# Kernel tuning notes

Measured on AMD Instinct MI355X. Metric: run time of the kernel, lower is better.

Reference implementation:

```python
import jax, jax.numpy as jnp
import numpy as np

B, S, D, H = 4, 2048, 1024, 16
HD = D // H  # head dim = 64


def setup_inputs() -> dict:
    key = jax.random.key(0)
    ks = jax.random.split(key, 11)
    sc = 1.0 / np.sqrt(D)
    return {
        "q": jax.random.normal(ks[0], (B, S, D), jnp.float32),
        "k": jax.random.normal(ks[1], (B, S, D), jnp.float32),
        "v": jax.random.normal(ks[2], (B, S, D), jnp.float32),
        "w_q": jax.random.normal(ks[3], (D, D), jnp.float32) * sc,
        "b_q": jnp.zeros((D,), jnp.float32),
        "w_k": jax.random.normal(ks[4], (D, D), jnp.float32) * sc,
        "b_k": jnp.zeros((D,), jnp.float32),
        "w_v": jax.random.normal(ks[5], (D, D), jnp.float32) * sc,
        "b_v": jnp.zeros((D,), jnp.float32),
        "w_fc": jax.random.normal(ks[6], (D, D), jnp.float32) * sc,
        "b_fc": jnp.zeros((D,), jnp.float32),
    }


def reference(q, k, v, w_q, b_q, w_k, b_k, w_v, b_v, w_fc, b_fc):
    scale = jnp.asarray(np.sqrt(HD), q.dtype)
    # QKV projections: [B,S,D] @ [D,D]^T (torch Linear: x @ W^T + b)
    Q = (q @ w_q.T + b_q).reshape(B, S, H, HD).transpose(0, 2, 1, 3)  # [B,H,S,HD]
    K = (k @ w_k.T + b_k).reshape(B, S, H, HD).transpose(0, 2, 1, 3)
    V = (v @ w_v.T + b_v).reshape(B, S, H, HD).transpose(0, 2, 1, 3)
    energy = jnp.einsum('bhqd,bhkd->bhqk', Q, K) / scale  # [B,H,S,S]
    attn = jax.nn.softmax(energy, axis=-1)  # dropout is identity in eval / p=0
    x = jnp.einsum('bhqk,bhkd->bhqd', attn, V)  # [B,H,S,HD]
    x = x.transpose(0, 2, 1, 3).reshape(B, S, D)
    return x @ w_fc.T + b_fc
```

## Files before the change

### kernel.cpp

```cpp
#include <hip/hip_runtime.h>
#include <stdint.h>

#define BN 4
#define SEQ 2048
#define DM 1024
#define NH 16
#define HD 64
#define ROWS (BN*SEQ)

typedef float  f32x4  __attribute__((ext_vector_type(4)));
typedef __bf16 bf16x8 __attribute__((ext_vector_type(8)));
typedef __bf16 bf16x4 __attribute__((ext_vector_type(4)));

#define QSCALE 0.18033688f

__device__ inline bf16x8 cvt8(const float* __restrict__ src) {
    float4 x0 = *(const float4*)src;
    float4 x1 = *(const float4*)(src + 4);
    bf16x8 r;
    r[0] = (__bf16)x0.x; r[1] = (__bf16)x0.y; r[2] = (__bf16)x0.z; r[3] = (__bf16)x0.w;
    r[4] = (__bf16)x1.x; r[5] = (__bf16)x1.y; r[6] = (__bf16)x1.z; r[7] = (__bf16)x1.w;
    return r;
}

__device__ inline void gl_lds16(const void* g, void* l) {
    __builtin_amdgcn_global_load_lds((const __attribute__((address_space(1))) uint32_t*)g,
                                     (__attribute__((address_space(3))) uint32_t*)l, 16, 0, 0);
}

__global__ __launch_bounds__(256) void cast3(
    const float* __restrict__ a0, const float* __restrict__ a1, const float* __restrict__ a2,
    __bf16* __restrict__ o0, __bf16* __restrict__ o1, __bf16* __restrict__ o2, int n8) {
    int t = blockIdx.x * 256 + threadIdx.x;
    if (t >= n8) return;
    const float* in = (blockIdx.y == 0) ? a0 : (blockIdx.y == 1) ? a1 : a2;
    __bf16* out     = (blockIdx.y == 0) ? o0 : (blockIdx.y == 1) ? o1 : o2;
    *(bf16x8*)&out[(size_t)t * 8] = cvt8(&in[(size_t)t * 8]);
}

__global__ __launch_bounds__(256) void cast4(
    const float* __restrict__ a0, const float* __restrict__ a1,
    const float* __restrict__ a2, const float* __restrict__ a3,
    __bf16* __restrict__ o0, __bf16* __restrict__ o1,
    __bf16* __restrict__ o2, __bf16* __restrict__ o3, int n8) {
    int t = blockIdx.x * 256 + threadIdx.x;
    if (t >= n8) return;
    const float* in = (blockIdx.y == 0) ? a0 : (blockIdx.y == 1) ? a1 : (blockIdx.y == 2) ? a2 : a3;
    __bf16* out     = (blockIdx.y == 0) ? o0 : (blockIdx.y == 1) ? o1 : (blockIdx.y == 2) ? o2 : o3;
    *(bf16x8*)&out[(size_t)t * 8] = cvt8(&in[(size_t)t * 8]);
}

#define GEMM_CORE_GLDS(Xp, Wp)                                                     \
    __shared__ __align__(16) __bf16 As[128 * 32];                                  \
    __shared__ __align__(16) __bf16 Bs[128 * 32];                                  \
    const int tid  = threadIdx.x;                                                  \
    const int lane = tid & 63;                                                     \
    const int wave = tid >> 6;                                                     \
    const int wm = (wave >> 1) * 64;                                               \
    const int wn = (wave & 1) * 64;                                                \
    const int c16 = lane & 15;                                                     \
    const int g8  = (lane >> 4) * 8;                                               \
    const int row0 = blockIdx.x * 128;                                             \
    const int col0 = blockIdx.y * 128;                                             \
    f32x4 acc[4][4] = {};                                                          \
    for (int k0 = 0; k0 < DM; k0 += 32) {                                          \
        __syncthreads();                                                           \
        _Pragma("unroll")                                                          \
        for (int h = 0; h < 2; h++) {                                              \
            int cidx = h * 256 + tid;                                              \
            gl_lds16(&Xp[(size_t)(row0 + (cidx >> 2)) * DM + k0 + (cidx & 3) * 8], \
                     &As[(size_t)(h * 256 + wave * 64) * 8]);                      \
            gl_lds16(&Wp[(size_t)(col0 + (cidx >> 2)) * DM + k0 + (cidx & 3) * 8], \
                     &Bs[(size_t)(h * 256 + wave * 64) * 8]);                      \
        }                                                                          \
        __syncthreads();                                                           \
        bf16x8 a[4], bfr[4];                                                       \
        _Pragma("unroll")                                                          \
        for (int i = 0; i < 4; i++) a[i]   = *(const bf16x8*)&As[(wm + i * 16 + c16) * 32 + g8]; \
        _Pragma("unroll")                                                          \
        for (int i = 0; i < 4; i++) bfr[i] = *(const bf16x8*)&Bs[(wn + i * 16 + c16) * 32 + g8]; \
        _Pragma("unroll")                                                          \
        for (int mi = 0; mi < 4; mi++)                                             \
            _Pragma("unroll")                                                      \
            for (int ni = 0; ni < 4; ni++)                                         \
                acc[mi][ni] = __builtin_amdgcn_mfma_f32_16x16x32_bf16(a[mi], bfr[ni], acc[mi][ni], 0, 0, 0); \
    }

__global__ __launch_bounds__(256) void gemm_qkv_f(
    const __bf16* __restrict__ qb, const __bf16* __restrict__ kb,
    const __bf16* __restrict__ vb,
    const __bf16* __restrict__ wqb, const __bf16* __restrict__ wkb,
    const __bf16* __restrict__ wvb,
    const float* __restrict__ bq, const float* __restrict__ bk,
    const float* __restrict__ bv,
    __bf16* __restrict__ Qp, __bf16* __restrict__ Kp, __bf16* __restrict__ Vt)
{
    const int z = blockIdx.z;
    const __bf16* X = (z == 0) ? qb : (z == 1) ? kb : vb;
    const __bf16* W = (z == 0) ? wqb : (z == 1) ? wkb : wvb;
    const float* bias = (z == 0) ? bq : (z == 1) ? bk : bv;

    GEMM_CORE_GLDS(X, W)

    if (z < 2) {
        __bf16* O = z ? Kp : Qp;
        const float qsc = z ? 1.0f : QSCALE;
        #pragma unroll
        for (int mi = 0; mi < 4; mi++) {
            int r0 = row0 + wm + mi * 16 + (lane >> 4) * 4;
            #pragma unroll
            for (int ni = 0; ni < 4; ni++) {
                int col = col0 + wn + ni * 16 + c16;
                float bsv = bias[col];
                int h = col >> 6, d = col & 63;
                #pragma unroll
                for (int i = 0; i < 4; i++) {
                    int r = r0 + i; int b = r >> 11, s = r & 2047;
                    O[((size_t)(b * NH + h) * SEQ + s) * HD + d] = (__bf16)((acc[mi][ni][i] + bsv) * qsc);
                }
            }
        }
    } else {
        #pragma unroll
        for (int mi = 0; mi < 4; mi++) {
            int r0 = row0 + wm + mi * 16 + (lane >> 4) * 4;
            #pragma unroll
            for (int ni = 0; ni < 4; ni++) {
                int col = col0 + wn + ni * 16 + c16;
                float bsv = bias[col];
                int h = col >> 6, d = col & 63;
                int b = r0 >> 11, s0 = r0 & 2047;
                size_t base = ((size_t)((b * NH + h) * HD + d)) * SEQ + s0;
                #pragma unroll
                for (int i = 0; i < 4; i++)
                    Vt[base + i] = (__bf16)(acc[mi][ni][i] + bsv);
            }
        }
    }
}

__global__ __launch_bounds__(256) void gemm_fc_f(
    const __bf16* __restrict__ Xc, const __bf16* __restrict__ Wfb,
    const float* __restrict__ bias, float* __restrict__ out)
{
    __shared__ __align__(16) __bf16 As[128 * 32];
    __shared__ __align__(16) __bf16 Bs[64 * 32];

    const int tid  = threadIdx.x;
    const int lane = tid & 63;
    const int wave = tid >> 6;
    const int wm = (wave >> 1) * 64;
    const int wn = (wave & 1) * 32;
    const int c16 = lane & 15;
    const int g8  = (lane >> 4) * 8;
    const int row0 = blockIdx.x * 128;
    const int col0 = blockIdx.y * 64;

    f32x4 acc[4][2] = {};
    for (int k0 = 0; k0 < DM; k0 += 32) {
        __syncthreads();
        #pragma unroll
        for (int h = 0; h < 2; h++) {
            int cidx = h * 256 + tid;
            gl_lds16(&Xc[(size_t)(row0 + (cidx >> 2)) * DM + k0 + (cidx & 3) * 8],
                     &As[(size_t)(h * 256 + wave * 64) * 8]);
        }
        gl_lds16(&Wfb[(size_t)(col0 + (tid >> 2)) * DM + k0 + (tid & 3) * 8],
                 &Bs[(size_t)(wave * 64) * 8]);
        __syncthreads();

        bf16x8 a[4], bfr[2];
        #pragma unroll
        for (int i = 0; i < 4; i++) a[i]   = *(const bf16x8*)&As[(wm + i * 16 + c16) * 32 + g8];
        #pragma unroll
        for (int i = 0; i < 2; i++) bfr[i] = *(const bf16x8*)&Bs[(wn + i * 16 + c16) * 32 + g8];
        #pragma unroll
        for (int mi = 0; mi < 4; mi++)
            #pragma unroll
            for (int ni = 0; ni < 2; ni++)
                acc[mi][ni] = __builtin_amdgcn_mfma_f32_16x16x32_bf16(a[mi], bfr[ni], acc[mi][ni], 0, 0, 0);
    }

    #pragma unroll
    for (int mi = 0; mi < 4; mi++) {
        int r0 = row0 + wm + mi * 16 + (lane >> 4) * 4;
        #pragma unroll
        for (int ni = 0; ni < 2; ni++) {
            int col = col0 + wn + ni * 16 + c16;
            float bsv = bias[col];
            #pragma unroll
            for (int i = 0; i < 4; i++)
                out[(size_t)(r0 + i) * DM + col] = acc[mi][ni][i] + bsv;
        }
    }
}

__global__ __launch_bounds__(256) void gemm_qk(
    const __bf16* __restrict__ qb, const __bf16* __restrict__ kb,
    const float* __restrict__ wqf, const float* __restrict__ wkf,
    const float* __restrict__ bq, const float* __restrict__ bk,
    __bf16* __restrict__ Qp, __bf16* __restrict__ Kp)
{
    const int z = blockIdx.z;
    const __bf16* X = z ? kb : qb;
    const float* W  = z ? wkf : wqf;
    const float* bias = z ? bk : bq;
    __bf16* O = z ? Kp : Qp;
    const float qsc = z ? 1.0f : QSCALE;

    __shared__ __align__(16) __bf16 As[128 * 32];
    __shared__ __align__(16) __bf16 Bs[128 * 32];

    const int tid  = threadIdx.x;
    const int lane = tid & 63;
    const int wave = tid >> 6;
    const int wm = (wave >> 1) * 64;
    const int wn = (wave & 1) * 64;
    const int c16 = lane & 15;
    const int g8  = (lane >> 4) * 8;
    const int row0 = blockIdx.x * 128;
    const int col0 = blockIdx.y * 128;
    const int brow = tid >> 1;
    const int bcc  = (tid & 1) * 16;

    f32x4 acc[4][4] = {};
    for (int k0 = 0; k0 < DM; k0 += 32) {
        __syncthreads();
        #pragma unroll
        for (int h = 0; h < 2; h++) {
            int cidx = h * 256 + tid;
            gl_lds16(&X[(size_t)(row0 + (cidx >> 2)) * DM + k0 + (cidx & 3) * 8],
                     &As[(size_t)(h * 256 + wave * 64) * 8]);
        }
        *(bf16x8*)&Bs[brow * 32 + bcc]     = cvt8(&W[(size_t)(col0 + brow) * DM + k0 + bcc]);
        *(bf16x8*)&Bs[brow * 32 + bcc + 8] = cvt8(&W[(size_t)(col0 + brow) * DM + k0 + bcc + 8]);
        __syncthreads();

        bf16x8 a[4], bfr[4];
        #pragma unroll
        for (int i = 0; i < 4; i++) a[i]   = *(const bf16x8*)&As[(wm + i * 16 + c16) * 32 + g8];
        #pragma unroll
        for (int i = 0; i < 4; i++) bfr[i] = *(const bf16x8*)&Bs[(wn + i * 16 + c16) * 32 + g8];
        #pragma unroll
        for (int mi = 0; mi < 4; mi++)
            #pragma unroll
            for (int ni = 0; ni < 4; ni++)
                acc[mi][ni] = __builtin_amdgcn_mfma_f32_16x16x32_bf16(a[mi], bfr[ni], acc[mi][ni], 0, 0, 0);
    }

    #pragma unroll
    for (int mi = 0; mi < 4; mi++) {
        int r0 = row0 + wm + mi * 16 + (lane >> 4) * 4;
        #pragma unroll
        for (int ni = 0; ni < 4; ni++) {
            int col = col0 + wn + ni * 16 + c16;
            float bsv = bias[col];
            int h = col >> 6, d = col & 63;
            #pragma unroll
            for (int i = 0; i < 4; i++) {
                int r = r0 + i; int b = r >> 11, s = r & 2047;
                O[((size_t)(b * NH + h) * SEQ + s) * HD + d] = (__bf16)((acc[mi][ni][i] + bsv) * qsc);
            }
        }
    }
}

__global__ __launch_bounds__(256) void gemm_v(
    const float* __restrict__ vf, const float* __restrict__ wvf,
    const float* __restrict__ bv, __bf16* __restrict__ Vt)
{
    __shared__ __align__(16) __bf16 As[128 * 32];
    __shared__ __align__(16) __bf16 Bs[128 * 32];

    const int tid  = threadIdx.x;
    const int lane = tid & 63;
    const int wave = tid >> 6;
    const int wm = (wave >> 1) * 64;
    const int wn = (wave & 1) * 64;
    const int c16 = lane & 15;
    const int g8  = (lane >> 4) * 8;
    const int row0 = blockIdx.x * 128;
    const int col0 = blockIdx.y * 128;
    const int brow = tid >> 1;
    const int bcc  = (tid & 1) * 16;

    f32x4 acc[4][4] = {};
    for (int k0 = 0; k0 < DM; k0 += 32) {
        __syncthreads();
        *(bf16x8*)&As[brow * 32 + bcc]     = cvt8(&vf[(size_t)(row0 + brow) * DM + k0 + bcc]);
        *(bf16x8*)&As[brow * 32 + bcc + 8] = cvt8(&vf[(size_t)(row0 + brow) * DM + k0 + bcc + 8]);
        *(bf16x8*)&Bs[brow * 32 + bcc]     = cvt8(&wvf[(size_t)(col0 + brow) * DM + k0 + bcc]);
        *(bf16x8*)&Bs[brow * 32 + bcc + 8] = cvt8(&wvf[(size_t)(col0 + brow) * DM + k0 + bcc + 8]);
        __syncthreads();

        bf16x8 a[4], bfr[4];
        #pragma unroll
        for (int i = 0; i < 4; i++) a[i]   = *(const bf16x8*)&As[(wm + i * 16 + c16) * 32 + g8];
        #pragma unroll
        for (int i = 0; i < 4; i++) bfr[i] = *(const bf16x8*)&Bs[(wn + i * 16 + c16) * 32 + g8];
        #pragma unroll
        for (int mi = 0; mi < 4; mi++)
            #pragma unroll
            for (int ni = 0; ni < 4; ni++)
                acc[mi][ni] = __builtin_amdgcn_mfma_f32_16x16x32_bf16(a[mi], bfr[ni], acc[mi][ni], 0, 0, 0);
    }

    #pragma unroll
    for (int mi = 0; mi < 4; mi++) {
        int r0 = row0 + wm + mi * 16 + (lane >> 4) * 4;
        #pragma unroll
        for (int ni = 0; ni < 4; ni++) {
            int col = col0 + wn + ni * 16 + c16;
            float bsv = bv[col];
            int h = col >> 6, d = col & 63;
            int b = r0 >> 11, s0 = r0 & 2047;
            size_t base = ((size_t)((b * NH + h) * HD + d)) * SEQ + s0;
            #pragma unroll
            for (int i = 0; i < 4; i++)
                Vt[base + i] = (__bf16)(acc[mi][ni][i] + bsv);
        }
    }
}

__global__ __launch_bounds__(256) void gemm_fc(
    const __bf16* __restrict__ Xc, const float* __restrict__ Wf,
    const float* __restrict__ bias, float* __restrict__ out)
{
    __shared__ __align__(16) __bf16 As[128 * 32];
    __shared__ __align__(16) __bf16 Bs[128 * 32];

    const int tid  = threadIdx.x;
    const int lane = tid & 63;
    const int wave = tid >> 6;
    const int wm = (wave >> 1) * 64;
    const int wn = (wave & 1) * 64;
    const int c16 = lane & 15;
    const int g8  = (lane >> 4) * 8;
    const int row0 = blockIdx.x * 128;
    const int col0 = blockIdx.y * 128;
    const int brow = tid >> 1;
    const int bcc  = (tid & 1) * 16;

    f32x4 acc[4][4] = {};
    for (int k0 = 0; k0 < DM; k0 += 32) {
        __syncthreads();
        #pragma unroll
        for (int h = 0; h < 2; h++) {
            int cidx = h * 256 + tid;
            gl_lds16(&Xc[(size_t)(row0 + (cidx >> 2)) * DM + k0 + (cidx & 3) * 8],
                     &As[(size_t)(h * 256 + wave * 64) * 8]);
        }
        *(bf16x8*)&Bs[brow * 32 + bcc]     = cvt8(&Wf[(size_t)(col0 + brow) * DM + k0 + bcc]);
        *(bf16x8*)&Bs[brow * 32 + bcc + 8] = cvt8(&Wf[(size_t)(col0 + brow) * DM + k0 + bcc + 8]);
        __syncthreads();

        bf16x8 a[4], bfr[4];
        #pragma unroll
        for (int i = 0; i < 4; i++) a[i]   = *(const bf16x8*)&As[(wm + i * 16 + c16) * 32 + g8];
        #pragma unroll
        for (int i = 0; i < 4; i++) bfr[i] = *(const bf16x8*)&Bs[(wn + i * 16 + c16) * 32 + g8];
        #pragma unroll
        for (int mi = 0; mi < 4; mi++)
            #pragma unroll
            for (int ni = 0; ni < 4; ni++)
                acc[mi][ni] = __builtin_amdgcn_mfma_f32_16x16x32_bf16(a[mi], bfr[ni], acc[mi][ni], 0, 0, 0);
    }

    #pragma unroll
    for (int mi = 0; mi < 4; mi++) {
        int r0 = row0 + wm + mi * 16 + (lane >> 4) * 4;
        #pragma unroll
        for (int ni = 0; ni < 4; ni++) {
            int col = col0 + wn + ni * 16 + c16;
            float bsv = bias[col];
            #pragma unroll
            for (int i = 0; i < 4; i++)
                out[(size_t)(r0 + i) * DM + col] = acc[mi][ni][i] + bsv;
        }
    }
}

__global__ __launch_bounds__(256, 4) void attn_kernel(
    const __bf16* __restrict__ Qp, const __bf16* __restrict__ Kp,
    const __bf16* __restrict__ Vt, __bf16* __restrict__ ctx)
{
    __shared__ __align__(16) __bf16 Ks[2][64 * 64];
    __shared__ __align__(16) __bf16 Vs[2][64 * 64];

    const int tid  = threadIdx.x;
    const int lane = tid & 63;
    const int w    = tid >> 6;
    const int bh   = blockIdx.x;
    const int q0   = blockIdx.y * 128 + w * 32;

    const __bf16* Qb = Qp + (size_t)bh * SEQ * HD;
    const __bf16* Kb = Kp + (size_t)bh * SEQ * HD;
    const __bf16* Vb = Vt + (size_t)bh * HD * SEQ;

    const int c16 = lane & 15;
    const int g   = lane >> 4;
    const int sw  = c16 & 7;

    bf16x8 qf[2][2];
    #pragma unroll
    for (int qs = 0; qs < 2; qs++)
        #pragma unroll
        for (int kc = 0; kc < 2; kc++)
            qf[qs][kc] = *(const bf16x8*)&Qb[(size_t)(q0 + qs * 16 + c16) * HD + kc * 32 + g * 8];

    float lp[2] = {0.f, 0.f};
    f32x4 o[4][2] = {};

    const int srow = (w * 16) + (lane >> 3);
    const int sj   = (lane & 7) ^ (lane >> 3);

    auto stage = [&](int kt, int buf) {
        const int k0 = kt * 64;
        #pragma unroll
        for (int h = 0; h < 2; h++) {
            int r = srow + h * 8;
            gl_lds16(&Kb[(size_t)(k0 + r) * HD + sj * 8], &Ks[buf][(size_t)(w * 16 + h * 8) * 64]);
            gl_lds16(&Vb[(size_t)r * SEQ + k0 + sj * 8],  &Vs[buf][(size_t)(w * 16 + h * 8) * 64]);
        }
    };

    const int NT = SEQ / 64;
    stage(0, 0);
    int cur = 0;

    for (int kt = 0; kt < NT; kt++) {
        __syncthreads();
        if (kt + 1 < NT) stage(kt + 1, cur ^ 1);

        const __bf16* ksb = &Ks[cur][0];
        const __bf16* vsb = &Vs[cur][0];

        f32x4 sc[4][2] = {};
        #pragma unroll
        for (int t = 0; t < 4; t++) {
            #pragma unroll
            for (int kc = 0; kc < 2; kc++) {
                bf16x8 kf = *(const bf16x8*)&ksb[(t * 16 + c16) * 64 + ((kc * 4 + g) ^ sw) * 8];
                sc[t][0] = __builtin_amdgcn_mfma_f32_16x16x32_bf16(kf, qf[0][kc], sc[t][0], 0, 0, 0);
                sc[t][1] = __builtin_amdgcn_mfma_f32_16x16x32_bf16(kf, qf[1][kc], sc[t][1], 0, 0, 0);
            }
        }

        bf16x8 pf[2][2];
        #pragma unroll
        for (int qs = 0; qs < 2; qs++) {
            float ps = 0.f;
            #pragma unroll
            for (int kc = 0; kc < 2; kc++) {
                bf16x8 pv8;
                #pragma unroll
                for (int i = 0; i < 4; i++) {
                    float pv = exp2f(sc[2 * kc][qs][i]);
                    ps += pv; pv8[i] = (__bf16)pv;
                }
                #pragma unroll
                for (int i = 0; i < 4; i++) {
                    float pv = exp2f(sc[2 * kc + 1][qs][i]);
                    ps += pv; pv8[4 + i] = (__bf16)pv;
                }
                pf[qs][kc] = pv8;
            }
            lp[qs] += ps;
        }

        #pragma unroll
        for (int t = 0; t < 4; t++) {
            #pragma unroll
            for (int kc = 0; kc < 2; kc++) {
                union { bf16x8 v8; bf16x4 v4[2]; } u;
                u.v4[0] = *(const bf16x4*)&vsb[(t * 16 + c16) * 64 + (((kc * 4 + (g >> 1)) ^ sw) * 8) + (g & 1) * 4];
                u.v4[1] = *(const bf16x4*)&vsb[(t * 16 + c16) * 64 + (((kc * 4 + 2 + (g >> 1)) ^ sw) * 8) + (g & 1) * 4];
                o[t][0] = __builtin_amdgcn_mfma_f32_16x16x32_bf16(u.v8, pf[0][kc], o[t][0], 0, 0, 0);
                o[t][1] = __builtin_amdgcn_mfma_f32_16x16x32_bf16(u.v8, pf[1][kc], o[t][1], 0, 0, 0);
            }
        }

        cur ^= 1;
    }

    const int hh = bh & (NH - 1);
    const int bb = bh >> 4;
    #pragma unroll
    for (int qs = 0; qs < 2; qs++) {
        float l = lp[qs];
        l += __shfl_xor(l, 16, 64);
        l += __shfl_xor(l, 32, 64);
        float inv = 1.f / l;
        int s = q0 + qs * 16 + c16;
        #pragma unroll
        for (int t = 0; t < 4; t++) {
            bf16x4 ov;
            #pragma unroll
            for (int i = 0; i < 4; i++) ov[i] = (__bf16)(o[t][qs][i] * inv);
            *(bf16x4*)&ctx[((size_t)(bb * SEQ + s)) * DM + hh * HD + t * 16 + g * 4] = ov;
        }
    }
}

extern "C" void kernel_launch(void* const* d_in, const int* in_sizes, int n_in,
                              void* d_out, int out_size, void* d_ws, size_t ws_size,
                              hipStream_t stream) {
    const float* q    = (const float*)d_in[0];
    const float* k    = (const float*)d_in[1];
    const float* v    = (const float*)d_in[2];
    const float* w_q  = (const float*)d_in[3];
    const float* b_q  = (const float*)d_in[4];
    const float* w_k  = (const float*)d_in[5];
    const float* b_k  = (const float*)d_in[6];
    const float* w_v  = (const float*)d_in[7];
    const float* b_v  = (const float*)d_in[8];
    const float* w_fc = (const float*)d_in[9];
    const float* b_fc = (const float*)d_in[10];
    float* out = (float*)d_out;

    __bf16* qb = (__bf16*)d_out;
    __bf16* kb = qb + (size_t)ROWS * DM;

    char* p = (char*)d_ws;
    auto alloc = [&](size_t bytes) { char* r = p; p += (bytes + 255) & ~(size_t)255; return r; };
    const size_t XSZ = (size_t)ROWS * DM * 2;
    const size_t WSZ = (size_t)DM * DM * 2;

    __bf16* Qp  = (__bf16*)alloc(XSZ);
    __bf16* Kp  = (__bf16*)alloc(XSZ);
    __bf16* Vt  = (__bf16*)alloc(XSZ);
    __bf16* ctx = (__bf16*)alloc(XSZ);

    const size_t base_need = (size_t)(p - (char*)d_ws);
    const size_t fast_need = base_need + 4 * (WSZ + 256);

    const int n8x = ROWS * DM / 8;
    const int n8w = DM * DM / 8;

    __bf16* vb = ctx;

    cast3<<<dim3(n8x / 256, 3), 256, 0, stream>>>(q, k, v, qb, kb, vb, n8x);

    if (ws_size >= fast_need) {
        __bf16* wqb  = (__bf16*)alloc(WSZ);
        __bf16* wkb  = (__bf16*)alloc(WSZ);
        __bf16* wvb  = (__bf16*)alloc(WSZ);
        __bf16* wfcb = (__bf16*)alloc(WSZ);

        cast4<<<dim3(n8w / 256, 4), 256, 0, stream>>>(
            w_q, w_k, w_v, w_fc, wqb, wkb, wvb, wfcb, n8w);

        gemm_qkv_f<<<dim3(ROWS / 128, DM / 128, 3), 256, 0, stream>>>(
            qb, kb, vb, wqb, wkb, wvb, b_q, b_k, b_v, Qp, Kp, Vt);

        attn_kernel<<<dim3(BN * NH, SEQ / 128), 256, 0, stream>>>(Qp, Kp, Vt, ctx);

        gemm_fc_f<<<dim3(ROWS / 128, DM / 64), 256, 0, stream>>>(ctx, wfcb, b_fc, out);
    } else {
        gemm_v<<<dim3(ROWS / 128, DM / 128), 256, 0, stream>>>(v, w_v, b_v, Vt);
        gemm_qk<<<dim3(ROWS / 128, DM / 128, 2), 256, 0, stream>>>(
            qb, kb, w_q, w_k, b_q, b_k, Qp, Kp);

        attn_kernel<<<dim3(BN * NH, SEQ / 128), 256, 0, stream>>>(Qp, Kp, Vt, ctx);

        gemm_fc<<<dim3(ROWS / 128, DM / 128), 256, 0, stream>>>(ctx, w_fc, b_fc, out);
    }
}
```

Before: 360.2 us.

## Software-pipeline attention: overlap next tile's QK MFMA with current softmax/PV

```diff
diff --git a/kernel.cpp b/kernel.cpp
--- a/kernel.cpp
+++ b/kernel.cpp
@@ -380,7 +380,61 @@
     }
 }
 
-__global__ __launch_bounds__(256, 4) void attn_kernel(
+#define QK_CLUSTER(SC, KSB)                                                        \
+    do {                                                                           \
+        _Pragma("unroll")                                                          \
+        for (int t_ = 0; t_ < 4; t_++) {                                           \
+            SC[t_][0] = (f32x4){0.f, 0.f, 0.f, 0.f};                               \
+            SC[t_][1] = (f32x4){0.f, 0.f, 0.f, 0.f};                               \
+        }                                                                          \
+        _Pragma("unroll")                                                          \
+        for (int t_ = 0; t_ < 4; t_++) {                                           \
+            _Pragma("unroll")                                                      \
+            for (int kc = 0; kc < 2; kc++) {                                       \
+                bf16x8 kf = *(const bf16x8*)&(KSB)[(t_ * 16 + c16) * 64 + ((kc * 4 + g) ^ sw) * 8]; \
+                SC[t_][0] = __builtin_amdgcn_mfma_f32_16x16x32_bf16(kf, qf[0][kc], SC[t_][0], 0, 0, 0); \
+                SC[t_][1] = __builtin_amdgcn_mfma_f32_16x16x32_bf16(kf, qf[1][kc], SC[t_][1], 0, 0, 0); \
+            }                                                                      \
+        }                                                                          \
+    } while (0)
+
+#define SOFTMAX_PV(SC, VSB)                                                        \
+    do {                                                                           \
+        bf16x8 pf[2][2];                                                           \
+        _Pragma("unroll")                                                          \
+        for (int qs = 0; qs < 2; qs++) {                                           \
+            float ps = 0.f;                                                        \
+            _Pragma("unroll")                                                      \
+            for (int kc = 0; kc < 2; kc++) {                                       \
+                bf16x8 pv8;                                                        \
+                _Pragma("unroll")                                                  \
+                for (int i = 0; i < 4; i++) {                                      \
+                    float pv = exp2f(SC[2 * kc][qs][i]);                           \
+                    ps += pv; pv8[i] = (__bf16)pv;                                 \
+                }                                                                  \
+                _Pragma("unroll")                                                  \
+                for (int i = 0; i < 4; i++) {                                      \
+                    float pv = exp2f(SC[2 * kc + 1][qs][i]);                       \
+                    ps += pv; pv8[4 + i] = (__bf16)pv;                             \
+                }                                                                  \
+                pf[qs][kc] = pv8;                                                  \
+            }                                                                      \
+            lp[qs] += ps;                                                          \
+        }                                                                          \
+        _Pragma("unroll")                                                          \
+        for (int t_ = 0; t_ < 4; t_++) {                                           \
+            _Pragma("unroll")                                                      \
+            for (int kc = 0; kc < 2; kc++) {                                       \
+                union { bf16x8 v8; bf16x4 v4[2]; } u;                              \
+                u.v4[0] = *(const bf16x4*)&(VSB)[(t_ * 16 + c16) * 64 + (((kc * 4 + (g >> 1)) ^ sw) * 8) + (g & 1) * 4]; \
+                u.v4[1] = *(const bf16x4*)&(VSB)[(t_ * 16 + c16) * 64 + (((kc * 4 + 2 + (g >> 1)) ^ sw) * 8) + (g & 1) * 4]; \
+                o[t_][0] = __builtin_amdgcn_mfma_f32_16x16x32_bf16(u.v8, pf[0][kc], o[t_][0], 0, 0, 0); \
+                o[t_][1] = __builtin_amdgcn_mfma_f32_16x16x32_bf16(u.v8, pf[1][kc], o[t_][1], 0, 0, 0); \
+            }                                                                      \
+        }                                                                          \
+    } while (0)
+
+__global__ __launch_bounds__(256) void attn_kernel(
     const __bf16* __restrict__ Qp, const __bf16* __restrict__ Kp,
     const __bf16* __restrict__ Vt, __bf16* __restrict__ ctx)
 {
@@ -410,77 +464,45 @@
 
     float lp[2] = {0.f, 0.f};
     f32x4 o[4][2] = {};
+    f32x4 scA[4][2], scB[4][2];
 
     const int srow = (w * 16) + (lane >> 3);
     const int sj   = (lane & 7) ^ (lane >> 3);
 
-    auto stage = [&](int kt, int buf) {
+    auto stageK = [&](int kt, int buf) {
         const int k0 = kt * 64;
         #pragma unroll
         for (int h = 0; h < 2; h++) {
             int r = srow + h * 8;
             gl_lds16(&Kb[(size_t)(k0 + r) * HD + sj * 8], &Ks[buf][(size_t)(w * 16 + h * 8) * 64]);
-            gl_lds16(&Vb[(size_t)r * SEQ + k0 + sj * 8],  &Vs[buf][(size_t)(w * 16 + h * 8) * 64]);
         }
     };
+    auto stageV = [&](int kt, int buf) {
+        const int k0 = kt * 64;
+        #pragma unroll
+        for (int h = 0; h < 2; h++) {
+            int r = srow + h * 8;
+            gl_lds16(&Vb[(size_t)r * SEQ + k0 + sj * 8], &Vs[buf][(size_t)(w * 16 + h * 8) * 64]);
+        }
+    };
 
     const int NT = SEQ / 64;
-    stage(0, 0);
-    int cur = 0;
-
-    for (int kt = 0; kt < NT; kt++) {
-        __syncthreads();
-        if (kt + 1 < NT) stage(kt + 1, cur ^ 1);
-
-        const __bf16* ksb = &Ks[cur][0];
-        const __bf16* vsb = &Vs[cur][0];
-
-        f32x4 sc[4][2] = {};
-        #pragma unroll
-        for (int t = 0; t < 4; t++) {
-            #pragma unroll
-            for (int kc = 0; kc < 2; kc++) {
-                bf16x8 kf = *(const bf16x8*)&ksb[(t * 16 + c16) * 64 + ((kc * 4 + g) ^ sw) * 8];
-                sc[t][0] = __builtin_amdgcn_mfma_f32_16x16x32_bf16(kf, qf[0][kc], sc[t][0], 0, 0, 0);
-                sc[t][1] = __builtin_amdgcn_mfma_f32_16x16x32_bf16(kf, qf[1][kc], sc[t][1], 0, 0, 0);
-            }
-        }
-
-        bf16x8 pf[2][2];
-        #pragma unroll
-        for (int qs = 0; qs < 2; qs++) {
-            float ps = 0.f;
-            #pragma unroll
-            for (int kc = 0; kc < 2; kc++) {
-                bf16x8 pv8;
-                #pragma unroll
-                for (int i = 0; i < 4; i++) {
-                    float pv = exp2f(sc[2 * kc][qs][i]);
-                    ps += pv; pv8[i] = (__bf16)pv;
-                }
-                #pragma unroll
-                for (int i = 0; i < 4; i++) {
-                    float pv = exp2f(sc[2 * kc + 1][qs][i]);
-                    ps += pv; pv8[4 + i] = (__bf16)pv;
-                }
-                pf[qs][kc] = pv8;
-            }
-            lp[qs] += ps;
-        }
-
-        #pragma unroll
-        for (int t = 0; t < 4; t++) {
-            #pragma unroll
-            for (int kc = 0; kc < 2; kc++) {
-                union { bf16x8 v8; bf16x4 v4[2]; } u;
-                u.v4[0] = *(const bf16x4*)&vsb[(t * 16 + c16) * 64 + (((kc * 4 + (g >> 1)) ^ sw) * 8) + (g & 1) * 4];
-                u.v4[1] = *(const bf16x4*)&vsb[(t * 16 + c16) * 64 + (((kc * 4 + 2 + (g >> 1)) ^ sw) * 8) + (g & 1) * 4];
-                o[t][0] = __builtin_amdgcn_mfma_f32_16x16x32_bf16(u.v8, pf[0][kc], o[t][0], 0, 0, 0);
-                o[t][1] = __builtin_amdgcn_mfma_f32_16x16x32_bf16(u.v8, pf[1][kc], o[t][1], 0, 0, 0);
-            }
-        }
-
-        cur ^= 1;
+    stageK(0, 0); stageV(0, 0); stageK(1, 1);
+    __syncthreads();
+    QK_CLUSTER(scA, &Ks[0][0]);
+
+    for (int t = 0; t < NT; t += 2) {
+        __syncthreads();
+        if (t + 1 < NT) QK_CLUSTER(scB, &Ks[1][0]);
+        if (t + 2 < NT) stageK(t + 2, 0);
+        if (t + 1 < NT) stageV(t + 1, 1);
+        SOFTMAX_PV(scA, &Vs[0][0]);
+
+        __syncthreads();
+        if (t + 2 < NT) QK_CLUSTER(scA, &Ks[0][0]);
+        if (t + 3 < NT) stageK(t + 3, 1);
+        if (t + 2 < NT) stageV(t + 2, 0);
+        if (t + 1 < NT) SOFTMAX_PV(scB, &Vs[1][0]);
     }
 
     const int hh = bh & (NH - 1);
```

Result: slower. 383.5 us (+6.5%).
